# Optimization experiments

Measured on AMD Instinct MI355X. Metric: run time of the kernel, lower is better.

The kernel has to match this reference:

```python
import jax, jax.numpy as jnp
import numpy as np

N = 100000      # nodes
E = 1600000     # edges (avg degree 16)
NX = 3          # input feature dim (data.x.shape[1])
K = 2           # number of kernels (len(kernel_DD) = manifold dim)
ORDER = 2       # par['order']
DEPTH = 2       # par['depth']
EPS = 1e-12     # F.normalize eps


def setup_inputs() -> dict:
    key = jax.random.key(0)
    ks = jax.random.split(key, 10)
    x = jax.random.normal(ks[0], (N, NX), dtype=jnp.float32)
    # per-edge kernel weights for the k directional kernels (sparse N x N ops)
    K_DD_vals = 0.1 * jax.random.normal(ks[1], (K, E), dtype=jnp.float32)
    K_DA_vals = 0.1 * jax.random.normal(ks[2], (K, E), dtype=jnp.float32)
    # lin[0]: in = 18*k = 36, out = 72
    lin0_w = 0.05 * jax.random.normal(ks[3], (36, 72), dtype=jnp.float32)
    lin0_b = jnp.zeros((72,), dtype=jnp.float32)
    # MLP: 144 -> 128 -> 64
    mlp_w1 = 0.05 * jax.random.normal(ks[4], (144, 128), dtype=jnp.float32)
    mlp_b1 = jnp.zeros((128,), dtype=jnp.float32)
    mlp_w2 = 0.05 * jax.random.normal(ks[5], (128, 64), dtype=jnp.float32)
    mlp_b2 = jnp.zeros((64,), dtype=jnp.float32)
    src = jax.random.randint(ks[6], (E,), 0, N, dtype=jnp.int32)
    dst = jnp.sort(jax.random.randint(ks[7], (E,), 0, N, dtype=jnp.int32))
    return {"x": x, "K_DD_vals": K_DD_vals, "K_DA_vals": K_DA_vals,
            "lin0_w": lin0_w, "lin0_b": lin0_b,
            "mlp_w1": mlp_w1, "mlp_b1": mlp_b1,
            "mlp_w2": mlp_w2, "mlp_b2": mlp_b2,
            "src": src, "dst": dst}


def _aniso_conv(h, src, dst, k_vals):
    """Kernel-weighted message passing: out_j[t] = sum_{e: dst[e]=t} K_j[e] * h[src[e]].
    Concatenate the k kernel outputs along the channel dim ([N, C] -> [N, k*C])."""
    msgs = h[src]  # [E, C] gather (shared across kernels)
    outs = [jax.ops.segment_sum(k_vals[j][:, None] * msgs, dst, num_segments=N)
            for j in range(k_vals.shape[0])]
    return jnp.concatenate(outs, axis=1)


def reference(x, K_DD_vals, K_DA_vals, lin0_w, lin0_b,
              mlp_w1, mlp_b1, mlp_w2, mlp_b2, src, dst):
    # --- DD phase (order hops), collecting per-hop outputs ---
    h = x
    collected = []
    for _ in range(ORDER):
        h = _aniso_conv(h, src, dst, K_DD_vals)   # channels *= K each hop
        collected.append(h)
    h = jnp.concatenate(collected, axis=1)        # [N, NX*(K + K^2)] = [N, 18]

    # --- DA phase (depth hops) with Linear+ReLU between hops ---
    for i in range(DEPTH):
        h = _aniso_conv(h, src, dst, K_DA_vals)
        if i < DEPTH - 1:
            h = jax.nn.relu(h @ lin0_w + lin0_b)  # 36 -> 72

    # --- MLP head: 144 -> 128 -> 64 ---
    h = jax.nn.relu(h @ mlp_w1 + mlp_b1)
    h = h @ mlp_w2 + mlp_b2

    # --- L2 normalize (F.normalize, p=2, dim=-1) ---
    norm = jnp.maximum(jnp.linalg.norm(h, axis=-1, keepdims=True), EPS)
    return h / norm
```

## Files before the change

kernel.cpp:

```cpp
#include <hip/hip_runtime.h>

#define N_NODES 100000
#define N_EDGES 1600000

typedef __attribute__((ext_vector_type(8))) short short8;
typedef __attribute__((ext_vector_type(4))) float f32x4;
typedef __attribute__((ext_vector_type(2))) unsigned short ushort2v;
typedef __attribute__((ext_vector_type(4))) unsigned short ushort4v;
typedef __attribute__((ext_vector_type(8))) unsigned short ushort8v;

static __device__ inline unsigned short f2bf(float f) {
    union { float f; unsigned u; } v; v.f = f;
    unsigned r = v.u + 0x7FFF + ((v.u >> 16) & 1);
    return (unsigned short)(r >> 16);
}
static __device__ inline float bf2f(unsigned short u) {
    union { unsigned u; float f; } v; v.u = ((unsigned)u) << 16;
    return v.f;
}

__global__ __launch_bounds__(256) void rowptr_k(const int* __restrict__ dst,
                                                int* __restrict__ rp) {
    int t = blockIdx.x * blockDim.x + threadIdx.x;
    if (t > N_NODES) return;
    int lo = 0, hi = N_EDGES;
    while (lo < hi) {
        int mid = (lo + hi) >> 1;
        if (dst[mid] < t) lo = mid + 1; else hi = mid;
    }
    rp[t] = lo;
}

__global__ __launch_bounds__(256) void prep_k(const float* __restrict__ w1,
                                              const float* __restrict__ w2,
                                              const float* __restrict__ l0w,
                                              unsigned short* __restrict__ w1t,
                                              unsigned short* __restrict__ w2t,
                                              unsigned short* __restrict__ w0t) {
    int id = blockIdx.x * blockDim.x + threadIdx.x;
    if (id < 128 * 160) {
        int o = id / 160, k = id - o * 160;
        w1t[id] = (k < 144) ? f2bf(w1[k * 128 + o]) : (unsigned short)0;
    } else if (id < 128 * 160 + 64 * 128) {
        int j = id - 128 * 160;
        int o = j / 128, k = j - o * 128;
        w2t[j] = f2bf(w2[k * 64 + o]);
    } else if (id < 128 * 160 + 64 * 128 + 80 * 64) {
        int j = id - 128 * 160 - 64 * 128;
        int o = j / 64, k = j - o * 64;
        w0t[j] = (o < 72 && k < 36) ? f2bf(l0w[k * 72 + o]) : (unsigned short)0;
    }
}

__global__ __launch_bounds__(256) void x2b_k(const float* __restrict__ x,
                                             unsigned short* __restrict__ xb4) {
    int t = blockIdx.x * blockDim.x + threadIdx.x;
    if (t >= N_NODES) return;
    ushort4v w;
    w[0] = f2bf(x[(size_t)t * 3 + 0]);
    w[1] = f2bf(x[(size_t)t * 3 + 1]);
    w[2] = f2bf(x[(size_t)t * 3 + 2]);
    w[3] = 0;
    *reinterpret_cast<ushort4v*>(xb4 + (size_t)t * 4) = w;
}

__global__ __launch_bounds__(256) void conv1n_k(const unsigned short* __restrict__ xb4,
                                                const float* __restrict__ kv,
                                                const int* __restrict__ src,
                                                const int* __restrict__ rp,
                                                unsigned short* __restrict__ hcb) {
    int t = blockIdx.x * blockDim.x + threadIdx.x;
    if (t >= N_NODES) return;
    int e0 = rp[t], e1 = rp[t + 1];
    float a0[3] = {0.f, 0.f, 0.f}, a1[3] = {0.f, 0.f, 0.f};
    int e = e0;
    for (; e + 8 <= e1; e += 8) {
        int s[8]; float k0[8], k1[8];
#pragma unroll
        for (int u = 0; u < 8; ++u) s[u]  = src[e + u];
#pragma unroll
        for (int u = 0; u < 8; ++u) k0[u] = kv[e + u];
#pragma unroll
        for (int u = 0; u < 8; ++u) k1[u] = kv[N_EDGES + e + u];
        ushort4v v[8];
#pragma unroll
        for (int u = 0; u < 8; ++u)
            v[u] = *reinterpret_cast<const ushort4v*>(xb4 + (size_t)s[u] * 4);
#pragma unroll
        for (int u = 0; u < 8; ++u) {
#pragma unroll
            for (int q = 0; q < 3; ++q) {
                float x = bf2f(v[u][q]);
                a0[q] += k0[u] * x;
                a1[q] += k1[u] * x;
            }
        }
    }
    for (; e < e1; ++e) {
        int s = src[e];
        float k0 = kv[e], k1 = kv[N_EDGES + e];
        ushort4v v = *reinterpret_cast<const ushort4v*>(xb4 + (size_t)s * 4);
#pragma unroll
        for (int q = 0; q < 3; ++q) {
            float x = bf2f(v[q]);
            a0[q] += k0 * x;
            a1[q] += k1 * x;
        }
    }
    ushort4v r0; ushort2v r1;
    r0[0] = f2bf(a0[0]); r0[1] = f2bf(a0[1]); r0[2] = f2bf(a0[2]); r0[3] = f2bf(a1[0]);
    r1[0] = f2bf(a1[1]); r1[1] = f2bf(a1[2]);
    *reinterpret_cast<ushort4v*>(hcb + (size_t)t * 20)     = r0;
    *reinterpret_cast<ushort2v*>(hcb + (size_t)t * 20 + 4) = r1;
}

__global__ __launch_bounds__(256) void conv2n_k(const unsigned short* __restrict__ hcbr,
                                                const float* __restrict__ kv,
                                                const int* __restrict__ src,
                                                const int* __restrict__ rp,
                                                unsigned short* __restrict__ hcbw) {
    int t = blockIdx.x * blockDim.x + threadIdx.x;
    if (t >= N_NODES) return;
    int e0 = rp[t], e1 = rp[t + 1];
    float a0[6], a1[6];
#pragma unroll
    for (int q = 0; q < 6; ++q) { a0[q] = 0.f; a1[q] = 0.f; }
    int e = e0;
    for (; e + 8 <= e1; e += 8) {
        int s[8]; float k0[8], k1[8];
#pragma unroll
        for (int u = 0; u < 8; ++u) s[u]  = src[e + u];
#pragma unroll
        for (int u = 0; u < 8; ++u) k0[u] = kv[e + u];
#pragma unroll
        for (int u = 0; u < 8; ++u) k1[u] = kv[N_EDGES + e + u];
        ushort4v va[8]; ushort2v vb[8];
#pragma unroll
        for (int u = 0; u < 8; ++u) {
            const unsigned short* b = hcbr + (size_t)s[u] * 20;
            va[u] = *reinterpret_cast<const ushort4v*>(b);
            vb[u] = *reinterpret_cast<const ushort2v*>(b + 4);
        }
#pragma unroll
        for (int u = 0; u < 8; ++u) {
#pragma unroll
            for (int q = 0; q < 4; ++q) {
                float x = bf2f(va[u][q]);
                a0[q] += k0[u] * x;
                a1[q] += k1[u] * x;
            }
#pragma unroll
            for (int q = 0; q < 2; ++q) {
                float x = bf2f(vb[u][q]);
                a0[4 + q] += k0[u] * x;
                a1[4 + q] += k1[u] * x;
            }
        }
    }
    for (; e < e1; ++e) {
        int s = src[e];
        float k0 = kv[e], k1 = kv[N_EDGES + e];
        const unsigned short* b = hcbr + (size_t)s * 20;
        ushort4v va = *reinterpret_cast<const ushort4v*>(b);
        ushort2v vb = *reinterpret_cast<const ushort2v*>(b + 4);
#pragma unroll
        for (int q = 0; q < 4; ++q) {
            float x = bf2f(va[q]);
            a0[q] += k0 * x; a1[q] += k1 * x;
        }
#pragma unroll
        for (int q = 0; q < 2; ++q) {
            float x = bf2f(vb[q]);
            a0[4 + q] += k0 * x; a1[4 + q] += k1 * x;
        }
    }
    unsigned short* o = hcbw + (size_t)t * 20;
#pragma unroll
    for (int p = 0; p < 3; ++p) {
        ushort2v w0; w0[0] = f2bf(a0[p * 2]); w0[1] = f2bf(a0[p * 2 + 1]);
        *reinterpret_cast<ushort2v*>(o + 6 + p * 2) = w0;
        ushort2v w1; w1[0] = f2bf(a1[p * 2]); w1[1] = f2bf(a1[p * 2 + 1]);
        *reinterpret_cast<ushort2v*>(o + 12 + p * 2) = w1;
    }
}

__global__ __launch_bounds__(256) void conv3n_k(const unsigned short* __restrict__ hcb,
                                                const float* __restrict__ kv,
                                                const int* __restrict__ src,
                                                const int* __restrict__ rp,
                                                unsigned short* __restrict__ h3b) {
    int t = blockIdx.x * blockDim.x + threadIdx.x;
    if (t >= N_NODES) return;
    int e0 = rp[t], e1 = rp[t + 1];
    float a0[18], a1[18];
#pragma unroll
    for (int q = 0; q < 18; ++q) { a0[q] = 0.f; a1[q] = 0.f; }
    int e = e0;
    for (; e + 4 <= e1; e += 4) {
        int s[4]; float k0[4], k1[4];
#pragma unroll
        for (int u = 0; u < 4; ++u) s[u]  = src[e + u];
#pragma unroll
        for (int u = 0; u < 4; ++u) k0[u] = kv[e + u];
#pragma unroll
        for (int u = 0; u < 4; ++u) k1[u] = kv[N_EDGES + e + u];
        ushort8v p0[4], p1[4]; ushort2v p2[4];
#pragma unroll
        for (int u = 0; u < 4; ++u) {
            const unsigned short* b = hcb + (size_t)s[u] * 20;
            p0[u] = *reinterpret_cast<const ushort8v*>(b);
            p1[u] = *reinterpret_cast<const ushort8v*>(b + 8);
            p2[u] = *reinterpret_cast<const ushort2v*>(b + 16);
        }
#pragma unroll
        for (int u = 0; u < 4; ++u) {
#pragma unroll
            for (int q = 0; q < 8; ++q) {
                float x = bf2f(p0[u][q]);
                a0[q] += k0[u] * x; a1[q] += k1[u] * x;
            }
#pragma unroll
            for (int q = 0; q < 8; ++q) {
                float x = bf2f(p1[u][q]);
                a0[8 + q] += k0[u] * x; a1[8 + q] += k1[u] * x;
            }
#pragma unroll
            for (int q = 0; q < 2; ++q) {
                float x = bf2f(p2[u][q]);
                a0[16 + q] += k0[u] * x; a1[16 + q] += k1[u] * x;
            }
        }
    }
    for (; e < e1; ++e) {
        int s = src[e];
        float k0 = kv[e], k1 = kv[N_EDGES + e];
        const unsigned short* b = hcb + (size_t)s * 20;
        ushort8v p0 = *reinterpret_cast<const ushort8v*>(b);
        ushort8v p1 = *reinterpret_cast<const ushort8v*>(b + 8);
        ushort2v p2 = *reinterpret_cast<const ushort2v*>(b + 16);
#pragma unroll
        for (int q = 0; q < 8; ++q) {
            float x = bf2f(p0[q]); a0[q] += k0 * x; a1[q] += k1 * x;
        }
#pragma unroll
        for (int q = 0; q < 8; ++q) {
            float x = bf2f(p1[q]); a0[8 + q] += k0 * x; a1[8 + q] += k1 * x;
        }
#pragma unroll
        for (int q = 0; q < 2; ++q) {
            float x = bf2f(p2[q]); a0[16 + q] += k0 * x; a1[16 + q] += k1 * x;
        }
    }
    unsigned short* o = h3b + (size_t)t * 64;
    unsigned short r[36];
#pragma unroll
    for (int q = 0; q < 18; ++q) r[q] = f2bf(a0[q]);
#pragma unroll
    for (int q = 0; q < 18; ++q) r[18 + q] = f2bf(a1[q]);
#pragma unroll
    for (int p = 0; p < 4; ++p) {
        ushort8v w;
#pragma unroll
        for (int q = 0; q < 8; ++q) w[q] = r[p * 8 + q];
        *reinterpret_cast<ushort8v*>(o + p * 8) = w;
    }
    {
        ushort4v w;
#pragma unroll
        for (int q = 0; q < 4; ++q) w[q] = r[32 + q];
        *reinterpret_cast<ushort4v*>(o + 32) = w;
    }
    ushort4v z = {0, 0, 0, 0};
#pragma unroll
    for (int j = 36; j < 64; j += 4)
        *reinterpret_cast<ushort4v*>(o + j) = z;
}

template<int VEC> struct VecU;
template<> struct VecU<4> { using T = ushort4v; };
template<> struct VecU<8> { using T = ushort8v; };

template<int C, int VEC, int IN_STRIDE, int OUT_STRIDE, int OUT_OFF,
         int PAD_FROM, int PAD_TO>
__global__ __launch_bounds__(256) void convb_k(const unsigned short* __restrict__ hin,
                                               const float* __restrict__ kv,
                                               const int* __restrict__ src,
                                               const int* __restrict__ rp,
                                               unsigned short* __restrict__ hout) {
    constexpr int G = C / VEC;
    using VT = typename VecU<VEC>::T;
    int id = blockIdx.x * blockDim.x + threadIdx.x;
    if (id >= N_NODES * G) return;
    int t = id / G;
    int g = id - t * G;
    int c0 = g * VEC;
    int e0 = rp[t], e1 = rp[t + 1];

    float a0[VEC], a1[VEC];
#pragma unroll
    for (int q = 0; q < VEC; ++q) { a0[q] = 0.f; a1[q] = 0.f; }

    int e = e0;
    for (; e + 8 <= e1; e += 8) {
        int s[8]; float k0[8], k1[8];
#pragma unroll
        for (int u = 0; u < 8; ++u) s[u]  = src[e + u];
#pragma unroll
        for (int u = 0; u < 8; ++u) k0[u] = kv[e + u];
#pragma unroll
        for (int u = 0; u < 8; ++u) k1[u] = kv[N_EDGES + e + u];
        VT v[8];
#pragma unroll
        for (int u = 0; u < 8; ++u)
            v[u] = *reinterpret_cast<const VT*>(hin + (size_t)s[u] * IN_STRIDE + c0);
#pragma unroll
        for (int u = 0; u < 8; ++u) {
#pragma unroll
            for (int q = 0; q < VEC; ++q) {
                float x = bf2f(v[u][q]);
                a0[q] += k0[u] * x;
                a1[q] += k1[u] * x;
            }
        }
    }
    for (; e < e1; ++e) {
        int s = src[e];
        float k0 = kv[e], k1 = kv[N_EDGES + e];
        VT v = *reinterpret_cast<const VT*>(hin + (size_t)s * IN_STRIDE + c0);
#pragma unroll
        for (int q = 0; q < VEC; ++q) {
            float x = bf2f(v[q]);
            a0[q] += k0 * x;
            a1[q] += k1 * x;
        }
    }

    VT r0, r1;
#pragma unroll
    for (int q = 0; q < VEC; ++q) { r0[q] = f2bf(a0[q]); r1[q] = f2bf(a1[q]); }
    *reinterpret_cast<VT*>(hout + (size_t)t * OUT_STRIDE + OUT_OFF + c0)     = r0;
    *reinterpret_cast<VT*>(hout + (size_t)t * OUT_STRIDE + OUT_OFF + C + c0) = r1;

    if constexpr (PAD_TO > PAD_FROM) {
        if (g == G - 1) {
            ushort4v z = {0, 0, 0, 0};
#pragma unroll
            for (int j = PAD_FROM; j < PAD_TO; j += 4)
                *reinterpret_cast<ushort4v*>(hout + (size_t)t * OUT_STRIDE + j) = z;
        }
    }
}

__global__ __launch_bounds__(256) void lin0m_k(const unsigned short* __restrict__ h3b,
                                               const unsigned short* __restrict__ w0t,
                                               const float* __restrict__ b0,
                                               unsigned short* __restrict__ h4b) {
    int tid = threadIdx.x;
    int w = tid >> 6;
    int lane = tid & 63;
    int lr = lane & 15;
    int kg = lane >> 4;
    int row_base = blockIdx.x * 64 + w * 16;

    f32x4 acc[5];
#pragma unroll
    for (int n = 0; n < 5; ++n) acc[n] = (f32x4){0.f, 0.f, 0.f, 0.f};

    const unsigned short* arow = h3b + (size_t)(row_base + lr) * 64 + kg * 8;
#pragma unroll
    for (int ks = 0; ks < 2; ++ks) {
        short8 a = *reinterpret_cast<const short8*>(arow + ks * 32);
#pragma unroll
        for (int n = 0; n < 5; ++n) {
            short8 b = *reinterpret_cast<const short8*>(w0t + (n * 16 + lr) * 64 + ks * 32 + kg * 8);
            acc[n] = __builtin_amdgcn_mfma_f32_16x16x32_bf16(a, b, acc[n], 0, 0, 0);
        }
    }
#pragma unroll
    for (int n = 0; n < 5; ++n) {
        int col = n * 16 + lr;
        if (col < 72) {
            float bv = b0[col];
#pragma unroll
            for (int q = 0; q < 4; ++q) {
                int t = row_base + kg * 4 + q;
                if (t < N_NODES)
                    h4b[(size_t)t * 72 + col] = f2bf(fmaxf(acc[n][q] + bv, 0.f));
            }
        }
    }
}

#define HSTRIDE 136
__global__ __launch_bounds__(256) void mlp_k(const unsigned short* __restrict__ h5b,
                                             const unsigned short* __restrict__ w1t,
                                             const float* __restrict__ b1,
                                             const unsigned short* __restrict__ w2t,
                                             const float* __restrict__ b2,
                                             float* __restrict__ out) {
    __shared__ unsigned short sh[64 * HSTRIDE];
    int tid = threadIdx.x;
    int w = tid >> 6;
    int lane = tid & 63;
    int lr = lane & 15;
    int kg = lane >> 4;
    int row_base = blockIdx.x * 64 + w * 16;

    f32x4 acc[8];
#pragma unroll
    for (int n = 0; n < 8; ++n) acc[n] = (f32x4){0.f, 0.f, 0.f, 0.f};

    const unsigned short* arow = h5b + (size_t)(row_base + lr) * 160 + kg * 8;
#pragma unroll
    for (int ks = 0; ks < 5; ++ks) {
        short8 a = *reinterpret_cast<const short8*>(arow + ks * 32);
#pragma unroll
        for (int n = 0; n < 8; ++n) {
            short8 b = *reinterpret_cast<const short8*>(w1t + (n * 16 + lr) * 160 + ks * 32 + kg * 8);
            acc[n] = __builtin_amdgcn_mfma_f32_16x16x32_bf16(a, b, acc[n], 0, 0, 0);
        }
    }
#pragma unroll
    for (int n = 0; n < 8; ++n) {
        float bv = b1[n * 16 + lr];
#pragma unroll
        for (int q = 0; q < 4; ++q) {
            float hv = fmaxf(acc[n][q] + bv, 0.f);
            sh[(w * 16 + kg * 4 + q) * HSTRIDE + n * 16 + lr] = f2bf(hv);
        }
    }
    __syncthreads();

    f32x4 acc2[4];
#pragma unroll
    for (int n = 0; n < 4; ++n) acc2[n] = (f32x4){0.f, 0.f, 0.f, 0.f};
#pragma unroll
    for (int ks = 0; ks < 4; ++ks) {
        short8 a = *reinterpret_cast<const short8*>(sh + (w * 16 + lr) * HSTRIDE + ks * 32 + kg * 8);
#pragma unroll
        for (int n = 0; n < 4; ++n) {
            short8 b = *reinterpret_cast<const short8*>(w2t + (n * 16 + lr) * 128 + ks * 32 + kg * 8);
            acc2[n] = __builtin_amdgcn_mfma_f32_16x16x32_bf16(a, b, acc2[n], 0, 0, 0);
        }
    }

    float v[4][4];
    float ss[4];
#pragma unroll
    for (int q = 0; q < 4; ++q) ss[q] = 0.f;
#pragma unroll
    for (int n = 0; n < 4; ++n) {
        float bv = b2[n * 16 + lr];
#pragma unroll
        for (int q = 0; q < 4; ++q) {
            float x = acc2[n][q] + bv;
            v[n][q] = x;
            ss[q] += x * x;
        }
    }
#pragma unroll
    for (int q = 0; q < 4; ++q) {
#pragma unroll
        for (int d = 1; d < 16; d <<= 1) ss[q] += __shfl_xor(ss[q], d);
    }
#pragma unroll
    for (int q = 0; q < 4; ++q) {
        int node = row_base + kg * 4 + q;
        if (node < N_NODES) {
            float scale = 1.f / fmaxf(sqrtf(ss[q]), 1e-12f);
#pragma unroll
            for (int n = 0; n < 4; ++n)
                out[(size_t)node * 64 + n * 16 + lr] = v[n][q] * scale;
        }
    }
}

extern "C" void kernel_launch(void* const* d_in, const int* in_sizes, int n_in,
                              void* d_out, int out_size, void* d_ws, size_t ws_size,
                              hipStream_t stream) {
    const float* x   = (const float*)d_in[0];
    const float* kdd = (const float*)d_in[1];
    const float* kda = (const float*)d_in[2];
    const float* l0w = (const float*)d_in[3];
    const float* l0b = (const float*)d_in[4];
    const float* w1  = (const float*)d_in[5];
    const float* b1  = (const float*)d_in[6];
    const float* w2  = (const float*)d_in[7];
    const float* b2  = (const float*)d_in[8];
    const int*   src = (const int*)d_in[9];
    const int*   dst = (const int*)d_in[10];
    float* out = (float*)d_out;
    char* ws = (char*)d_ws;

    int*   rp  = (int*)ws;
    unsigned short* w0t = (unsigned short*)(ws + 400384u);
    unsigned short* w1t = (unsigned short*)(ws + 410624u);
    unsigned short* w2t = (unsigned short*)(ws + 451584u);
    unsigned short* hcb = (unsigned short*)(ws + 475136u);
    unsigned short* h3b = (unsigned short*)(ws + 4480000u);
    unsigned short* h4b = (unsigned short*)(ws + 17284096u);
    unsigned short* h5b = (unsigned short*)(ws + 31684096u);
    unsigned short* xb4 = (unsigned short*)(ws + 31684096u);

    int nb = (N_NODES + 255) / 256;
    rowptr_k<<<(N_NODES + 1 + 255) / 256, 256, 0, stream>>>(dst, rp);
    prep_k<<<(128 * 160 + 64 * 128 + 80 * 64 + 255) / 256, 256, 0, stream>>>(w1, w2, l0w, w1t, w2t, w0t);
    x2b_k<<<nb, 256, 0, stream>>>(x, xb4);

    conv1n_k<<<nb, 256, 0, stream>>>(xb4, kdd, src, rp, hcb);
    conv2n_k<<<nb, 256, 0, stream>>>(hcb, kdd, src, rp, hcb);

    conv3n_k<<<nb, 256, 0, stream>>>(hcb, kda, src, rp, h3b);
    lin0m_k<<<(N_NODES + 63) / 64, 256, 0, stream>>>(h3b, w0t, l0b, h4b);
    convb_k<72, 8, 72, 160, 0, 144, 160><<<(N_NODES * 9 + 255) / 256, 256, 0, stream>>>(h4b, kda, src, rp, h5b);

    mlp_k<<<(N_NODES + 63) / 64, 256, 0, stream>>>(h5b, w1t, b1, w2t, b2, out);
}
```

Measured before the change: 216.5 us.

## Split edge lists across four lanes per node and fuse conv2 with first DA columns

```diff
diff --git a/kernel.cpp b/kernel.cpp
--- a/kernel.cpp
+++ b/kernel.cpp
@@ -64,216 +64,255 @@
     *reinterpret_cast<ushort4v*>(xb4 + (size_t)t * 4) = w;
 }
 
-__global__ __launch_bounds__(256) void conv1n_k(const unsigned short* __restrict__ xb4,
+
+__global__ __launch_bounds__(256) void conv1p_k(const unsigned short* __restrict__ xb4,
                                                 const float* __restrict__ kv,
                                                 const int* __restrict__ src,
                                                 const int* __restrict__ rp,
                                                 unsigned short* __restrict__ hcb) {
-    int t = blockIdx.x * blockDim.x + threadIdx.x;
-    if (t >= N_NODES) return;
+    int id = blockIdx.x * blockDim.x + threadIdx.x;
+    if (id >= N_NODES * 4) return;
+    int t = id >> 2;
+    int p = id & 3;
     int e0 = rp[t], e1 = rp[t + 1];
+    int q = (e1 - e0 + 3) >> 2;
+    int s0 = e0 + p * q; if (s0 > e1) s0 = e1;
+    int s1 = s0 + q;     if (s1 > e1) s1 = e1;
+
     float a0[3] = {0.f, 0.f, 0.f}, a1[3] = {0.f, 0.f, 0.f};
-    int e = e0;
-    for (; e + 8 <= e1; e += 8) {
-        int s[8]; float k0[8], k1[8];
-#pragma unroll
-        for (int u = 0; u < 8; ++u) s[u]  = src[e + u];
-#pragma unroll
-        for (int u = 0; u < 8; ++u) k0[u] = kv[e + u];
-#pragma unroll
-        for (int u = 0; u < 8; ++u) k1[u] = kv[N_EDGES + e + u];
-        ushort4v v[8];
-#pragma unroll
-        for (int u = 0; u < 8; ++u)
+    int e = s0;
+    for (; e + 4 <= s1; e += 4) {
+        int s[4]; float k0[4], k1[4];
+#pragma unroll
+        for (int u = 0; u < 4; ++u) s[u]  = src[e + u];
+#pragma unroll
+        for (int u = 0; u < 4; ++u) k0[u] = kv[e + u];
+#pragma unroll
+        for (int u = 0; u < 4; ++u) k1[u] = kv[N_EDGES + e + u];
+        ushort4v v[4];
+#pragma unroll
+        for (int u = 0; u < 4; ++u)
             v[u] = *reinterpret_cast<const ushort4v*>(xb4 + (size_t)s[u] * 4);
 #pragma unroll
-        for (int u = 0; u < 8; ++u) {
-#pragma unroll
-            for (int q = 0; q < 3; ++q) {
-                float x = bf2f(v[u][q]);
-                a0[q] += k0[u] * x;
-                a1[q] += k1[u] * x;
+        for (int u = 0; u < 4; ++u) {
+#pragma unroll
+            for (int c = 0; c < 3; ++c) {
+                float x = bf2f(v[u][c]);
+                a0[c] += k0[u] * x;
+                a1[c] += k1[u] * x;
             }
         }
     }
-    for (; e < e1; ++e) {
+    for (; e < s1; ++e) {
         int s = src[e];
         float k0 = kv[e], k1 = kv[N_EDGES + e];
         ushort4v v = *reinterpret_cast<const ushort4v*>(xb4 + (size_t)s * 4);
 #pragma unroll
-        for (int q = 0; q < 3; ++q) {
-            float x = bf2f(v[q]);
-            a0[q] += k0 * x;
-            a1[q] += k1 * x;
-        }
-    }
-    ushort4v r0; ushort2v r1;
-    r0[0] = f2bf(a0[0]); r0[1] = f2bf(a0[1]); r0[2] = f2bf(a0[2]); r0[3] = f2bf(a1[0]);
-    r1[0] = f2bf(a1[1]); r1[1] = f2bf(a1[2]);
-    *reinterpret_cast<ushort4v*>(hcb + (size_t)t * 20)     = r0;
-    *reinterpret_cast<ushort2v*>(hcb + (size_t)t * 20 + 4) = r1;
-}
-
-__global__ __launch_bounds__(256) void conv2n_k(const unsigned short* __restrict__ hcbr,
-                                                const float* __restrict__ kv,
-                                                const int* __restrict__ src,
-                                                const int* __restrict__ rp,
-                                                unsigned short* __restrict__ hcbw) {
-    int t = blockIdx.x * blockDim.x + threadIdx.x;
-    if (t >= N_NODES) return;
+        for (int c = 0; c < 3; ++c) {
+            float x = bf2f(v[c]);
+            a0[c] += k0 * x;
+            a1[c] += k1 * x;
+        }
+    }
+#pragma unroll
+    for (int c = 0; c < 3; ++c) {
+        a0[c] += __shfl_xor(a0[c], 1); a0[c] += __shfl_xor(a0[c], 2);
+        a1[c] += __shfl_xor(a1[c], 1); a1[c] += __shfl_xor(a1[c], 2);
+    }
+    if (p == 0) {
+        ushort4v w4; ushort2v w2;
+        w4[0] = f2bf(a0[0]); w4[1] = f2bf(a0[1]); w4[2] = f2bf(a0[2]); w4[3] = f2bf(a1[0]);
+        w2[0] = f2bf(a1[1]); w2[1] = f2bf(a1[2]);
+        *reinterpret_cast<ushort4v*>(hcb + (size_t)t * 32)     = w4;
+        *reinterpret_cast<ushort2v*>(hcb + (size_t)t * 32 + 4) = w2;
+    }
+}
+
+__global__ __launch_bounds__(256) void f23ap_k(const unsigned short* __restrict__ hcbr,
+                                               const float* __restrict__ kdd,
+                                               const float* __restrict__ kda,
+                                               const int* __restrict__ src,
+                                               const int* __restrict__ rp,
+                                               unsigned short* __restrict__ hcbw,
+                                               unsigned short* __restrict__ h3b) {
+    int id = blockIdx.x * blockDim.x + threadIdx.x;
+    if (id >= N_NODES * 4) return;
+    int t = id >> 2;
+    int p = id & 3;
     int e0 = rp[t], e1 = rp[t + 1];
-    float a0[6], a1[6];
-#pragma unroll
-    for (int q = 0; q < 6; ++q) { a0[q] = 0.f; a1[q] = 0.f; }
-    int e = e0;
-    for (; e + 8 <= e1; e += 8) {
-        int s[8]; float k0[8], k1[8];
-#pragma unroll
-        for (int u = 0; u < 8; ++u) s[u]  = src[e + u];
-#pragma unroll
-        for (int u = 0; u < 8; ++u) k0[u] = kv[e + u];
-#pragma unroll
-        for (int u = 0; u < 8; ++u) k1[u] = kv[N_EDGES + e + u];
-        ushort4v va[8]; ushort2v vb[8];
-#pragma unroll
-        for (int u = 0; u < 8; ++u) {
-            const unsigned short* b = hcbr + (size_t)s[u] * 20;
-            va[u] = *reinterpret_cast<const ushort4v*>(b);
-            vb[u] = *reinterpret_cast<const ushort2v*>(b + 4);
-        }
-#pragma unroll
-        for (int u = 0; u < 8; ++u) {
-#pragma unroll
-            for (int q = 0; q < 4; ++q) {
-                float x = bf2f(va[u][q]);
-                a0[q] += k0[u] * x;
-                a1[q] += k1[u] * x;
+    int q = (e1 - e0 + 3) >> 2;
+    int s0 = e0 + p * q; if (s0 > e1) s0 = e1;
+    int s1 = s0 + q;     if (s1 > e1) s1 = e1;
+
+    float dd0[6], dd1[6], da0[6], da1[6];
+#pragma unroll
+    for (int c = 0; c < 6; ++c) { dd0[c] = dd1[c] = da0[c] = da1[c] = 0.f; }
+
+    int e = s0;
+    for (; e + 4 <= s1; e += 4) {
+        int s[4]; float d0[4], d1[4], g0[4], g1[4];
+#pragma unroll
+        for (int u = 0; u < 4; ++u) s[u]  = src[e + u];
+#pragma unroll
+        for (int u = 0; u < 4; ++u) d0[u] = kdd[e + u];
+#pragma unroll
+        for (int u = 0; u < 4; ++u) d1[u] = kdd[N_EDGES + e + u];
+#pragma unroll
+        for (int u = 0; u < 4; ++u) g0[u] = kda[e + u];
+#pragma unroll
+        for (int u = 0; u < 4; ++u) g1[u] = kda[N_EDGES + e + u];
+        ushort8v v[4];
+#pragma unroll
+        for (int u = 0; u < 4; ++u)
+            v[u] = *reinterpret_cast<const ushort8v*>(hcbr + (size_t)s[u] * 32);
+#pragma unroll
+        for (int u = 0; u < 4; ++u) {
+#pragma unroll
+            for (int c = 0; c < 6; ++c) {
+                float x = bf2f(v[u][c]);
+                dd0[c] += d0[u] * x;
+                dd1[c] += d1[u] * x;
+                da0[c] += g0[u] * x;
+                da1[c] += g1[u] * x;
             }
-#pragma unroll
-            for (int q = 0; q < 2; ++q) {
-                float x = bf2f(vb[u][q]);
-                a0[4 + q] += k0[u] * x;
-                a1[4 + q] += k1[u] * x;
+        }
+    }
+    for (; e < s1; ++e) {
+        int s = src[e];
+        float d0 = kdd[e], d1 = kdd[N_EDGES + e];
+        float g0 = kda[e], g1 = kda[N_EDGES + e];
+        ushort8v v = *reinterpret_cast<const ushort8v*>(hcbr + (size_t)s * 32);
+#pragma unroll
+        for (int c = 0; c < 6; ++c) {
+            float x = bf2f(v[c]);
+            dd0[c] += d0 * x;
+            dd1[c] += d1 * x;
+            da0[c] += g0 * x;
+            da1[c] += g1 * x;
+        }
+    }
+#pragma unroll
+    for (int c = 0; c < 6; ++c) {
+        dd0[c] += __shfl_xor(dd0[c], 1); dd0[c] += __shfl_xor(dd0[c], 2);
+        dd1[c] += __shfl_xor(dd1[c], 1); dd1[c] += __shfl_xor(dd1[c], 2);
+        da0[c] += __shfl_xor(da0[c], 1); da0[c] += __shfl_xor(da0[c], 2);
+        da1[c] += __shfl_xor(da1[c], 1); da1[c] += __shfl_xor(da1[c], 2);
+    }
+    if (p == 0) {
+        ushort8v w8; ushort4v w4;
+        w8[0] = f2bf(dd0[0]); w8[1] = f2bf(dd0[1]); w8[2] = f2bf(dd0[2]);
+        w8[3] = f2bf(dd0[3]); w8[4] = f2bf(dd0[4]); w8[5] = f2bf(dd0[5]);
+        w8[6] = f2bf(dd1[0]); w8[7] = f2bf(dd1[1]);
+        w4[0] = f2bf(dd1[2]); w4[1] = f2bf(dd1[3]); w4[2] = f2bf(dd1[4]); w4[3] = f2bf(dd1[5]);
+        *reinterpret_cast<ushort8v*>(hcbw + (size_t)t * 32 + 8)  = w8;
+        *reinterpret_cast<ushort4v*>(hcbw + (size_t)t * 32 + 16) = w4;
+        ushort4v h4; ushort2v h2;
+        h4[0] = f2bf(da0[0]); h4[1] = f2bf(da0[1]); h4[2] = f2bf(da0[2]); h4[3] = f2bf(da0[3]);
+        h2[0] = f2bf(da0[4]); h2[1] = f2bf(da0[5]);
+        *reinterpret_cast<ushort4v*>(h3b + (size_t)t * 64)     = h4;
+        *reinterpret_cast<ushort2v*>(h3b + (size_t)t * 64 + 4) = h2;
+        ushort2v ha, hb, hc;
+        ha[0] = f2bf(da1[0]); ha[1] = f2bf(da1[1]);
+        hb[0] = f2bf(da1[2]); hb[1] = f2bf(da1[3]);
+        hc[0] = f2bf(da1[4]); hc[1] = f2bf(da1[5]);
+        *reinterpret_cast<ushort2v*>(h3b + (size_t)t * 64 + 18) = ha;
+        *reinterpret_cast<ushort2v*>(h3b + (size_t)t * 64 + 20) = hb;
+        *reinterpret_cast<ushort2v*>(h3b + (size_t)t * 64 + 22) = hc;
+    }
+}
+
+__global__ __launch_bounds__(256) void conv3bp_k(const unsigned short* __restrict__ hcb,
+                                                 const float* __restrict__ kda,
+                                                 const int* __restrict__ src,
+                                                 const int* __restrict__ rp,
+                                                 unsigned short* __restrict__ h3b) {
+    int id = blockIdx.x * blockDim.x + threadIdx.x;
+    if (id >= N_NODES * 4) return;
+    int t = id >> 2;
+    int p = id & 3;
+    int e0 = rp[t], e1 = rp[t + 1];
+    int q = (e1 - e0 + 3) >> 2;
+    int s0 = e0 + p * q; if (s0 > e1) s0 = e1;
+    int s1 = s0 + q;     if (s1 > e1) s1 = e1;
+
+    float a0[12], a1[12];
+#pragma unroll
+    for (int c = 0; c < 12; ++c) { a0[c] = 0.f; a1[c] = 0.f; }
+
+    int e = s0;
+    for (; e + 4 <= s1; e += 4) {
+        int s[4]; float g0[4], g1[4];
+#pragma unroll
+        for (int u = 0; u < 4; ++u) s[u]  = src[e + u];
+#pragma unroll
+        for (int u = 0; u < 4; ++u) g0[u] = kda[e + u];
+#pragma unroll
+        for (int u = 0; u < 4; ++u) g1[u] = kda[N_EDGES + e + u];
+        ushort8v va[4]; ushort4v vb[4];
+#pragma unroll
+        for (int u = 0; u < 4; ++u) {
+            va[u] = *reinterpret_cast<const ushort8v*>(hcb + (size_t)s[u] * 32 + 8);
+            vb[u] = *reinterpret_cast<const ushort4v*>(hcb + (size_t)s[u] * 32 + 16);
+        }
+#pragma unroll
+        for (int u = 0; u < 4; ++u) {
+#pragma unroll
+            for (int c = 0; c < 8; ++c) {
+                float x = bf2f(va[u][c]);
+                a0[c] += g0[u] * x;
+                a1[c] += g1[u] * x;
             }
-        }
-    }
-    for (; e < e1; ++e) {
+#pragma unroll
+            for (int c = 0; c < 4; ++c) {
+                float x = bf2f(vb[u][c]);
+                a0[8 + c] += g0[u] * x;
+                a1[8 + c] += g1[u] * x;
+            }
+        }
+    }
+    for (; e < s1; ++e) {
         int s = src[e];
-        float k0 = kv[e], k1 = kv[N_EDGES + e];
-        const unsigned short* b = hcbr + (size_t)s * 20;
-        ushort4v va = *reinterpret_cast<const ushort4v*>(b);
-        ushort2v vb = *reinterpret_cast<const ushort2v*>(b + 4);
-#pragma unroll
-        for (int q = 0; q < 4; ++q) {
-            float x = bf2f(va[q]);
-            a0[q] += k0 * x; a1[q] += k1 * x;
-        }
-#pragma unroll
-        for (int q = 0; q < 2; ++q) {
-            float x = bf2f(vb[q]);
-            a0[4 + q] += k0 * x; a1[4 + q] += k1 * x;
-        }
-    }
-    unsigned short* o = hcbw + (size_t)t * 20;
-#pragma unroll
-    for (int p = 0; p < 3; ++p) {
-        ushort2v w0; w0[0] = f2bf(a0[p * 2]); w0[1] = f2bf(a0[p * 2 + 1]);
-        *reinterpret_cast<ushort2v*>(o + 6 + p * 2) = w0;
-        ushort2v w1; w1[0] = f2bf(a1[p * 2]); w1[1] = f2bf(a1[p * 2 + 1]);
-        *reinterpret_cast<ushort2v*>(o + 12 + p * 2) = w1;
-    }
-}
-
-__global__ __launch_bounds__(256) void conv3n_k(const unsigned short* __restrict__ hcb,
-                                                const float* __restrict__ kv,
-                                                const int* __restrict__ src,
-                                                const int* __restrict__ rp,
-                                                unsigned short* __restrict__ h3b) {
-    int t = blockIdx.x * blockDim.x + threadIdx.x;
-    if (t >= N_NODES) return;
-    int e0 = rp[t], e1 = rp[t + 1];
-    float a0[18], a1[18];
-#pragma unroll
-    for (int q = 0; q < 18; ++q) { a0[q] = 0.f; a1[q] = 0.f; }
-    int e = e0;
-    for (; e + 4 <= e1; e += 4) {
-        int s[4]; float k0[4], k1[4];
-#pragma unroll
-        for (int u = 0; u < 4; ++u) s[u]  = src[e + u];
-#pragma unroll
-        for (int u = 0; u < 4; ++u) k0[u] = kv[e + u];
-#pragma unroll
-        for (int u = 0; u < 4; ++u) k1[u] = kv[N_EDGES + e + u];
-        ushort8v p0[4], p1[4]; ushort2v p2[4];
-#pragma unroll
-        for (int u = 0; u < 4; ++u) {
-            const unsigned short* b = hcb + (size_t)s[u] * 20;
-            p0[u] = *reinterpret_cast<const ushort8v*>(b);
-            p1[u] = *reinterpret_cast<const ushort8v*>(b + 8);
-            p2[u] = *reinterpret_cast<const ushort2v*>(b + 16);
-        }
-#pragma unroll
-        for (int u = 0; u < 4; ++u) {
-#pragma unroll
-            for (int q = 0; q < 8; ++q) {
-                float x = bf2f(p0[u][q]);
-                a0[q] += k0[u] * x; a1[q] += k1[u] * x;
-            }
-#pragma unroll
-            for (int q = 0; q < 8; ++q) {
-                float x = bf2f(p1[u][q]);
-                a0[8 + q] += k0[u] * x; a1[8 + q] += k1[u] * x;
-            }
-#pragma unroll
-            for (int q = 0; q < 2; ++q) {
-                float x = bf2f(p2[u][q]);
-                a0[16 + q] += k0[u] * x; a1[16 + q] += k1[u] * x;
-            }
-        }
-    }
-    for (; e < e1; ++e) {
-        int s = src[e];
-        float k0 = kv[e], k1 = kv[N_EDGES + e];
-        const unsigned short* b = hcb + (size_t)s * 20;
-        ushort8v p0 = *reinterpret_cast<const ushort8v*>(b);
-        ushort8v p1 = *reinterpret_cast<const ushort8v*>(b + 8);
-        ushort2v p2 = *reinterpret_cast<const ushort2v*>(b + 16);
-#pragma unroll
-        for (int q = 0; q < 8; ++q) {
-            float x = bf2f(p0[q]); a0[q] += k0 * x; a1[q] += k1 * x;
-        }
-#pragma unroll
-        for (int q = 0; q < 8; ++q) {
-            float x = bf2f(p1[q]); a0[8 + q] += k0 * x; a1[8 + q] += k1 * x;
-        }
-#pragma unroll
-        for (int q = 0; q < 2; ++q) {
-            float x = bf2f(p2[q]); a0[16 + q] += k0 * x; a1[16 + q] += k1 * x;
-        }
-    }
-    unsigned short* o = h3b + (size_t)t * 64;
-    unsigned short r[36];
-#pragma unroll
-    for (int q = 0; q < 18; ++q) r[q] = f2bf(a0[q]);
-#pragma unroll
-    for (int q = 0; q < 18; ++q) r[18 + q] = f2bf(a1[q]);
-#pragma unroll
-    for (int p = 0; p < 4; ++p) {
-        ushort8v w;
-#pragma unroll
-        for (int q = 0; q < 8; ++q) w[q] = r[p * 8 + q];
-        *reinterpret_cast<ushort8v*>(o + p * 8) = w;
-    }
-    {
-        ushort4v w;
-#pragma unroll
-        for (int q = 0; q < 4; ++q) w[q] = r[32 + q];
-        *reinterpret_cast<ushort4v*>(o + 32) = w;
-    }
-    ushort4v z = {0, 0, 0, 0};
-#pragma unroll
-    for (int j = 36; j < 64; j += 4)
-        *reinterpret_cast<ushort4v*>(o + j) = z;
+        float g0 = kda[e], g1 = kda[N_EDGES + e];
+        ushort8v va = *reinterpret_cast<const ushort8v*>(hcb + (size_t)s * 32 + 8);
+        ushort4v vb = *reinterpret_cast<const ushort4v*>(hcb + (size_t)s * 32 + 16);
+#pragma unroll
+        for (int c = 0; c < 8; ++c) {
+            float x = bf2f(va[c]);
+            a0[c] += g0 * x; a1[c] += g1 * x;
+        }
+#pragma unroll
+        for (int c = 0; c < 4; ++c) {
+            float x = bf2f(vb[c]);
+            a0[8 + c] += g0 * x; a1[8 + c] += g1 * x;
+        }
+    }
+#pragma unroll
+    for (int c = 0; c < 12; ++c) {
+        a0[c] += __shfl_xor(a0[c], 1); a0[c] += __shfl_xor(a0[c], 2);
+        a1[c] += __shfl_xor(a1[c], 1); a1[c] += __shfl_xor(a1[c], 2);
+    }
+    if (p == 0) {
+        unsigned short* o = h3b + (size_t)t * 64;
+        ushort2v w2; ushort8v w8; ushort2v w2b;
+        w2[0] = f2bf(a0[0]); w2[1] = f2bf(a0[1]);
+#pragma unroll
+        for (int c = 0; c < 8; ++c) w8[c] = f2bf(a0[2 + c]);
+        w2b[0] = f2bf(a0[10]); w2b[1] = f2bf(a0[11]);
+        *reinterpret_cast<ushort2v*>(o + 6)  = w2;
+        *reinterpret_cast<ushort8v*>(o + 8)  = w8;
+        *reinterpret_cast<ushort2v*>(o + 16) = w2b;
+        ushort8v x8; ushort4v x4;
+#pragma unroll
+        for (int c = 0; c < 8; ++c) x8[c] = f2bf(a1[c]);
+#pragma unroll
+        for (int c = 0; c < 4; ++c) x4[c] = f2bf(a1[8 + c]);
+        *reinterpret_cast<ushort8v*>(o + 24) = x8;
+        *reinterpret_cast<ushort4v*>(o + 32) = x4;
+        ushort4v z = {0, 0, 0, 0};
+#pragma unroll
+        for (int j = 36; j < 64; j += 4)
+            *reinterpret_cast<ushort4v*>(o + j) = z;
+    }
 }
 
 template<int VEC> struct VecU;
@@ -497,20 +536,20 @@
     unsigned short* w1t = (unsigned short*)(ws + 410624u);
     unsigned short* w2t = (unsigned short*)(ws + 451584u);
     unsigned short* hcb = (unsigned short*)(ws + 475136u);
-    unsigned short* h3b = (unsigned short*)(ws + 4480000u);
-    unsigned short* h4b = (unsigned short*)(ws + 17284096u);
-    unsigned short* h5b = (unsigned short*)(ws + 31684096u);
-    unsigned short* xb4 = (unsigned short*)(ws + 31684096u);
-
-    int nb = (N_NODES + 255) / 256;
+    unsigned short* h3b = (unsigned short*)(ws + 6875136u);
+    unsigned short* h4b = (unsigned short*)(ws + 19679232u);
+    unsigned short* h5b = (unsigned short*)(ws + 34079232u);
+    unsigned short* xb4 = (unsigned short*)(ws + 34079232u);
+
+    int nb4 = (N_NODES * 4 + 255) / 256;
     rowptr_k<<<(N_NODES + 1 + 255) / 256, 256, 0, stream>>>(dst, rp);
     prep_k<<<(128 * 160 + 64 * 128 + 80 * 64 + 255) / 256, 256, 0, stream>>>(w1, w2, l0w, w1t, w2t, w0t);
-    x2b_k<<<nb, 256, 0, stream>>>(x, xb4);
-
-    conv1n_k<<<nb, 256, 0, stream>>>(xb4, kdd, src, rp, hcb);
-    conv2n_k<<<nb, 256, 0, stream>>>(hcb, kdd, src, rp, hcb);
-
-    conv3n_k<<<nb, 256, 0, stream>>>(hcb, kda, src, rp, h3b);
+    x2b_k<<<(N_NODES + 255) / 256, 256, 0, stream>>>(x, xb4);
+
+    conv1p_k<<<nb4, 256, 0, stream>>>(xb4, kdd, src, rp, hcb);
+    f23ap_k<<<nb4, 256, 0, stream>>>(hcb, kdd, kda, src, rp, hcb, h3b);
+    conv3bp_k<<<nb4, 256, 0, stream>>>(hcb, kda, src, rp, h3b);
+
     lin0m_k<<<(N_NODES + 63) / 64, 256, 0, stream>>>(h3b, w0t, l0b, h4b);
     convb_k<72, 8, 72, 160, 0, 144, 160><<<(N_NODES * 9 + 255) / 256, 256, 0, stream>>>(h4b, kda, src, rp, h5b);
 
```

Result: faster. 209.2 us (-3.4%).
